# Performance work log

Hardware: AMD Instinct MI355X
Metric: run time of the kernel (lower is better)

The kernel has to match this reference:

```python
import jax, jax.numpy as jnp
import numpy as np

N_NODES = 100000
N_EDGES = 3200000
IN_DIM = 512
HEADS = 4
C1 = 8   # per-head channels, conv1
C2 = 4   # per-head channels, conv2
OUT_DIM = 10
NUM_GRAPHS = 64
NEG_SLOPE = 0.2  # PyG GATConv default


def setup_inputs() -> dict:
    key = jax.random.key(0)
    ks = jax.random.split(key, 16)
    s = lambda fan_in: 1.0 / np.sqrt(fan_in)
    inp = {
        "x": jax.random.normal(ks[0], (N_NODES, IN_DIM), jnp.float32),
        "edge_index": jax.random.randint(ks[1], (2, N_EDGES), 0, N_NODES, jnp.int32),
        "batch": jnp.sort(jax.random.randint(ks[2], (N_NODES,), 0, NUM_GRAPHS, jnp.int32)),
        # conv1 params
        "W1": jax.random.normal(ks[3], (IN_DIM, HEADS * C1), jnp.float32) * s(IN_DIM),
        "a1_src": jax.random.normal(ks[4], (HEADS, C1), jnp.float32) * s(C1),
        "a1_dst": jax.random.normal(ks[5], (HEADS, C1), jnp.float32) * s(C1),
        "b1": jnp.zeros((HEADS * C1,), jnp.float32),
        # conv2 params
        "W2": jax.random.normal(ks[6], (HEADS * C1, HEADS * C2), jnp.float32) * s(HEADS * C1),
        "a2_src": jax.random.normal(ks[7], (HEADS, C2), jnp.float32) * s(C2),
        "a2_dst": jax.random.normal(ks[8], (HEADS, C2), jnp.float32) * s(C2),
        "b2": jnp.zeros((HEADS * C2,), jnp.float32),
        # final linear
        "Wfc": jax.random.normal(ks[9], (HEADS * C2, OUT_DIM), jnp.float32) * s(HEADS * C2),
        "bfc": jnp.zeros((OUT_DIM,), jnp.float32),
    }
    return inp


def gat_conv(x, src, dst, W, a_src, a_dst, b):
    # x: [N, F]; src/dst: [E'] (self-loops already appended)
    N = x.shape[0]
    H, C = a_src.shape
    h = (x @ W).reshape(N, H, C)                      # per-node linear transform
    e_src = (h * a_src).sum(-1)                        # [N, H]
    e_dst = (h * a_dst).sum(-1)                        # [N, H]
    e = jax.nn.leaky_relu(e_src[src] + e_dst[dst], NEG_SLOPE)  # [E', H]
    # segment softmax over incoming edges of each destination node
    m = jax.ops.segment_max(e, dst, num_segments=N)    # [N, H]
    p = jnp.exp(e - m[dst])
    denom = jax.ops.segment_sum(p, dst, num_segments=N)
    alpha = p / denom[dst]                             # [E', H]
    out = jax.ops.segment_sum(h[src] * alpha[:, :, None], dst, num_segments=N)
    return out.reshape(N, H * C) + b


def reference(x, edge_index, batch, W1, a1_src, a1_dst, b1,
              W2, a2_src, a2_dst, b2, Wfc, bfc):
    N = x.shape[0]
    loops = jnp.arange(N, dtype=edge_index.dtype)      # PyG GATConv adds self-loops
    src = jnp.concatenate([edge_index[0], loops])
    dst = jnp.concatenate([edge_index[1], loops])

    h = jax.nn.relu(gat_conv(x, src, dst, W1, a1_src, a1_dst, b1))
    h = jax.nn.relu(gat_conv(h, src, dst, W2, a2_src, a2_dst, b2))

    # global mean pool over graph ids
    sums = jax.ops.segment_sum(h, batch, num_segments=NUM_GRAPHS)
    cnts = jax.ops.segment_sum(jnp.ones((N,), h.dtype), batch, num_segments=NUM_GRAPHS)
    pooled = sums / jnp.maximum(cnts, 1.0)[:, None]    # [G, H*C2]

    return pooled @ Wfc + bfc                          # [G, OUT_DIM]
```

## Files before the change

### kernel.cpp

```cpp
#include <hip/hip_runtime.h>
#include <hip/hip_bf16.h>

#define HEADS 4
#define NEG 0.2f
#define SHIFT 7
#define BKT 128

typedef float fv4 __attribute__((ext_vector_type(4)));
typedef unsigned short uv4 __attribute__((ext_vector_type(4)));
typedef unsigned short uv8 __attribute__((ext_vector_type(8)));

static __device__ __forceinline__ unsigned short f2bf(float f) {
  unsigned u = __float_as_uint(f);
  u += 0x7FFFu + ((u >> 16) & 1u);
  return (unsigned short)(u >> 16);
}
static __device__ __forceinline__ float bf2f(unsigned short h) {
  return __uint_as_float((unsigned)h << 16);
}

__global__ __launch_bounds__(256) void k_bin(const int* __restrict__ ei, int E,
                                             int K, int CAP,
                                             int* __restrict__ cursor,
                                             int* __restrict__ bins) {
  __shared__ int lcnt[1024];
  __shared__ int gbase[1024];
  const int t = threadIdx.x;
  const int nb = (E + 4095) >> 12;
  for (int batch = blockIdx.x; batch < nb; batch += gridDim.x) {
    const int e0 = batch << 12;
    for (int i = t; i < K; i += 256) lcnt[i] = 0;
    __syncthreads();
    int sreg[16], dreg[16], rank[16];
#pragma unroll
    for (int j = 0; j < 16; ++j) {
      int e = e0 + j * 256 + t;
      dreg[j] = -1;
      if (e < E) {
        sreg[j] = ei[e];
        dreg[j] = ei[E + e];
        rank[j] = atomicAdd(&lcnt[dreg[j] >> SHIFT], 1);
      }
    }
    __syncthreads();
    for (int i = t; i < K; i += 256)
      gbase[i] = (lcnt[i] > 0) ? atomicAdd(&cursor[i], lcnt[i]) : 0;
    __syncthreads();
#pragma unroll
    for (int j = 0; j < 16; ++j) {
      if (dreg[j] >= 0) {
        int b = dreg[j] >> SHIFT;
        int slot = gbase[b] + rank[j];
        if (slot < CAP)
          bins[(size_t)b * CAP + slot] = (sreg[j] << SHIFT) | (dreg[j] & (BKT - 1));
      }
    }
    __syncthreads();
  }
}

__global__ __launch_bounds__(256) void k_sort(int* __restrict__ bins,
                                              const int* __restrict__ cursor,
                                              int CAP, int N,
                                              int* __restrict__ rowbase,
                                              int* __restrict__ deg) {
  __shared__ int ebuf[6144];
  __shared__ int sbuf[6144];
  __shared__ int hist[BKT], pre[BKT], cur[BKT];
  const int b = blockIdx.x;
  const int base = b << SHIFT;
  const int t = threadIdx.x;
  int total = cursor[b]; if (total > CAP) total = CAP;
  int* gsrc = bins + (size_t)b * CAP;
  for (int i = t; i < total; i += 256) ebuf[i] = gsrc[i];
  if (t < BKT) hist[t] = 0;
  __syncthreads();
  for (int i = t; i < total; i += 256) atomicAdd(&hist[ebuf[i] & (BKT - 1)], 1);
  __syncthreads();
  if (t < BKT) pre[t] = hist[t];
  __syncthreads();
  for (int off = 1; off < BKT; off <<= 1) {
    int v = (t < BKT && t >= off) ? pre[t - off] : 0;
    __syncthreads();
    if (t < BKT) pre[t] += v;
    __syncthreads();
  }
  if (t < BKT) {
    int ex = pre[t] - hist[t];
    cur[t] = ex;
    int n = base + t;
    if (n < N) { rowbase[n] = b * CAP + ex; deg[n] = hist[t]; }
  }
  __syncthreads();
  for (int i = t; i < total; i += 256) {
    int pk = ebuf[i];
    int r = atomicAdd(&cur[pk & (BKT - 1)], 1);
    sbuf[r] = pk >> SHIFT;
  }
  __syncthreads();
  for (int i = t; i < total; i += 256) gsrc[i] = sbuf[i];
}

__global__ __launch_bounds__(256) void k_gemm1(const float* __restrict__ x,
                                               const float* __restrict__ W,
                                               const float* __restrict__ a1s,
                                               const float* __restrict__ a1d,
                                               unsigned short* __restrict__ g1b,
                                               float* __restrict__ e1s,
                                               float* __restrict__ e1d, int N) {
  __shared__ __align__(16) float xs[64][68];
  __shared__ __align__(16) float ws[64][32];
  const int t = threadIdx.x;
  const int n0 = blockIdx.x * 64;
  const int nl = t >> 2;
  const int cg = t & 3;
  float acc[8];
#pragma unroll
  for (int j = 0; j < 8; ++j) acc[j] = 0.f;
  const int r = t >> 4;
  const int kk = (t & 15) << 2;
  fv4 xr[4];
  float4 wr0, wr1;
#pragma unroll
  for (int i = 0; i < 4; ++i) {
    int gn = n0 + r + i * 16;
    fv4 v = {0.f, 0.f, 0.f, 0.f};
    if (gn < N) v = __builtin_nontemporal_load((const fv4*)(x + (size_t)gn * 512 + kk));
    xr[i] = v;
  }
  wr0 = ((const float4*)W)[t];
  wr1 = ((const float4*)W)[t + 256];
  for (int kc = 0; kc < 512; kc += 64) {
    __syncthreads();
#pragma unroll
    for (int i = 0; i < 4; ++i) *(fv4*)(&xs[r + i * 16][kk]) = xr[i];
    ((float4*)ws)[t] = wr0;
    ((float4*)ws)[t + 256] = wr1;
    __syncthreads();
    const int kn = kc + 64;
    if (kn < 512) {
#pragma unroll
      for (int i = 0; i < 4; ++i) {
        int gn = n0 + r + i * 16;
        fv4 v = {0.f, 0.f, 0.f, 0.f};
        if (gn < N) v = __builtin_nontemporal_load((const fv4*)(x + (size_t)gn * 512 + kn + kk));
        xr[i] = v;
      }
      wr0 = ((const float4*)(W + kn * 32))[t];
      wr1 = ((const float4*)(W + kn * 32))[t + 256];
    }
#pragma unroll
    for (int k = 0; k < 64; ++k) {
      float xv = xs[nl][k];
      float4 w0 = *(const float4*)(&ws[k][cg * 8]);
      float4 w1 = *(const float4*)(&ws[k][cg * 8 + 4]);
      acc[0] = fmaf(xv, w0.x, acc[0]);
      acc[1] = fmaf(xv, w0.y, acc[1]);
      acc[2] = fmaf(xv, w0.z, acc[2]);
      acc[3] = fmaf(xv, w0.w, acc[3]);
      acc[4] = fmaf(xv, w1.x, acc[4]);
      acc[5] = fmaf(xv, w1.y, acc[5]);
      acc[6] = fmaf(xv, w1.z, acc[6]);
      acc[7] = fmaf(xv, w1.w, acc[7]);
    }
  }
  int gn = n0 + nl;
  if (gn < N) {
    uv8 pk;
#pragma unroll
    for (int j = 0; j < 8; ++j) pk[j] = f2bf(acc[j]);
    *(uv8*)(g1b + (size_t)gn * 32 + cg * 8) = pk;
    const float* as = a1s + cg * 8;
    const float* ad = a1d + cg * 8;
    float s = 0.f, d = 0.f;
#pragma unroll
    for (int j = 0; j < 8; ++j) { s = fmaf(acc[j], as[j], s); d = fmaf(acc[j], ad[j], d); }
    e1s[gn * 4 + cg] = s;
    e1d[gn * 4 + cg] = d;
  }
}

__global__ __launch_bounds__(256) void k_agg1(const int* __restrict__ rowbase,
                                              const int* __restrict__ deg,
                                              const int* __restrict__ csr,
                                              const float* __restrict__ e1s,
                                              const float* __restrict__ e1d,
                                              const unsigned short* __restrict__ g1b,
                                              const float* __restrict__ b1,
                                              float* __restrict__ h1, int N) {
  int gid = blockIdx.x * blockDim.x + threadIdx.x;
  if (gid >= N * 8) return;
  int n = gid >> 3, cg = gid & 7, hd = cg >> 1;
  float edn = e1d[n * 4 + hd];
  float s = e1s[n * 4 + hd] + edn;
  float p = __expf(s > 0.f ? s : NEG * s);
  uv4 hv = *(const uv4*)(g1b + (size_t)n * 32 + cg * 4);
  float4 acc = make_float4(p * bf2f(hv.x), p * bf2f(hv.y), p * bf2f(hv.z), p * bf2f(hv.w));
  float den = p;
  int beg = rowbase[n], len = deg[n];
  const int* row = csr + beg;
  int i = 0;
  for (; i + 4 <= len; i += 4) {
    int s0 = row[i], s1 = row[i + 1], s2 = row[i + 2], s3 = row[i + 3];
    float ea = e1s[s0 * 4 + hd] + edn;
    float eb = e1s[s1 * 4 + hd] + edn;
    float ec = e1s[s2 * 4 + hd] + edn;
    float ed = e1s[s3 * 4 + hd] + edn;
    uv4 v0 = *(const uv4*)(g1b + (size_t)s0 * 32 + cg * 4);
    uv4 v1 = *(const uv4*)(g1b + (size_t)s1 * 32 + cg * 4);
    uv4 v2 = *(const uv4*)(g1b + (size_t)s2 * 32 + cg * 4);
    uv4 v3 = *(const uv4*)(g1b + (size_t)s3 * 32 + cg * 4);
    float p0 = __expf(ea > 0.f ? ea : NEG * ea);
    float p1 = __expf(eb > 0.f ? eb : NEG * eb);
    float p2 = __expf(ec > 0.f ? ec : NEG * ec);
    float p3 = __expf(ed > 0.f ? ed : NEG * ed);
    acc.x = fmaf(p0, bf2f(v0.x), acc.x);
    acc.y = fmaf(p0, bf2f(v0.y), acc.y);
    acc.z = fmaf(p0, bf2f(v0.z), acc.z);
    acc.w = fmaf(p0, bf2f(v0.w), acc.w);
    acc.x = fmaf(p1, bf2f(v1.x), acc.x);
    acc.y = fmaf(p1, bf2f(v1.y), acc.y);
    acc.z = fmaf(p1, bf2f(v1.z), acc.z);
    acc.w = fmaf(p1, bf2f(v1.w), acc.w);
    acc.x = fmaf(p2, bf2f(v2.x), acc.x);
    acc.y = fmaf(p2, bf2f(v2.y), acc.y);
    acc.z = fmaf(p2, bf2f(v2.z), acc.z);
    acc.w = fmaf(p2, bf2f(v2.w), acc.w);
    acc.x = fmaf(p3, bf2f(v3.x), acc.x);
    acc.y = fmaf(p3, bf2f(v3.y), acc.y);
    acc.z = fmaf(p3, bf2f(v3.z), acc.z);
    acc.w = fmaf(p3, bf2f(v3.w), acc.w);
    den += p0 + p1 + p2 + p3;
  }
  for (; i < len; ++i) {
    int s0 = row[i];
    float ea = e1s[s0 * 4 + hd] + edn;
    float p0 = __expf(ea > 0.f ? ea : NEG * ea);
    uv4 v0 = *(const uv4*)(g1b + (size_t)s0 * 32 + cg * 4);
    acc.x = fmaf(p0, bf2f(v0.x), acc.x);
    acc.y = fmaf(p0, bf2f(v0.y), acc.y);
    acc.z = fmaf(p0, bf2f(v0.z), acc.z);
    acc.w = fmaf(p0, bf2f(v0.w), acc.w);
    den += p0;
  }
  float inv = 1.f / den;
  const float* bp = b1 + cg * 4;
  float4 o;
  o.x = fmaxf(fmaf(acc.x, inv, bp[0]), 0.f);
  o.y = fmaxf(fmaf(acc.y, inv, bp[1]), 0.f);
  o.z = fmaxf(fmaf(acc.z, inv, bp[2]), 0.f);
  o.w = fmaxf(fmaf(acc.w, inv, bp[3]), 0.f);
  *(float4*)(h1 + (size_t)gid * 4) = o;
}

__global__ __launch_bounds__(256) void k_gemm2(const float* __restrict__ h1,
                                               const float* __restrict__ W2,
                                               const float* __restrict__ a2s_,
                                               const float* __restrict__ a2d_,
                                               unsigned short* __restrict__ g2b,
                                               float* __restrict__ e2s,
                                               float* __restrict__ e2d, int N) {
  __shared__ __align__(16) float hs[64][36];
  __shared__ __align__(16) float ws[32][16];
  const int t = threadIdx.x;
  const int n0 = blockIdx.x * 64;
  {
    int row = t >> 3, c4 = (t & 7) * 4;
#pragma unroll
    for (int i = 0; i < 2; ++i) {
      int rr = row + i * 32;
      int gn = n0 + rr;
      float4 v = make_float4(0.f, 0.f, 0.f, 0.f);
      if (gn < N) v = *(const float4*)(h1 + (size_t)gn * 32 + c4);
      *(float4*)(&hs[rr][c4]) = v;
    }
    if (t < 128) ((float4*)ws)[t] = ((const float4*)W2)[t];
  }
  __syncthreads();
  const int nl = t >> 2, cg = t & 3;
  float acc[4] = {0.f, 0.f, 0.f, 0.f};
#pragma unroll
  for (int k = 0; k < 32; ++k) {
    float xv = hs[nl][k];
    float4 w = *(const float4*)(&ws[k][cg * 4]);
    acc[0] = fmaf(xv, w.x, acc[0]);
    acc[1] = fmaf(xv, w.y, acc[1]);
    acc[2] = fmaf(xv, w.z, acc[2]);
    acc[3] = fmaf(xv, w.w, acc[3]);
  }
  int gn = n0 + nl;
  if (gn < N) {
    uv4 pk;
#pragma unroll
    for (int j = 0; j < 4; ++j) pk[j] = f2bf(acc[j]);
    *(uv4*)(g2b + (size_t)gn * 16 + cg * 4) = pk;
    const float* as = a2s_ + cg * 4;
    const float* ad = a2d_ + cg * 4;
    e2s[gn * 4 + cg] = acc[0] * as[0] + acc[1] * as[1] + acc[2] * as[2] + acc[3] * as[3];
    e2d[gn * 4 + cg] = acc[0] * ad[0] + acc[1] * ad[1] + acc[2] * ad[2] + acc[3] * ad[3];
  }
}

__global__ __launch_bounds__(256) void k_agg2(const int* __restrict__ rowbase,
                                              const int* __restrict__ deg,
                                              const int* __restrict__ csr,
                                              const float* __restrict__ e2s,
                                              const float* __restrict__ e2d,
                                              const unsigned short* __restrict__ g2b,
                                              const float* __restrict__ b2,
                                              float* __restrict__ h2, int N) {
  int gid = blockIdx.x * blockDim.x + threadIdx.x;
  if (gid >= N * 4) return;
  int n = gid >> 2, hd = gid & 3;
  float edn = e2d[n * 4 + hd];
  float s = e2s[n * 4 + hd] + edn;
  float p = __expf(s > 0.f ? s : NEG * s);
  uv4 hv = *(const uv4*)(g2b + (size_t)n * 16 + hd * 4);
  float4 acc = make_float4(p * bf2f(hv.x), p * bf2f(hv.y), p * bf2f(hv.z), p * bf2f(hv.w));
  float den = p;
  int beg = rowbase[n], len = deg[n];
  const int* row = csr + beg;
  int i = 0;
  for (; i + 4 <= len; i += 4) {
    int s0 = row[i], s1 = row[i + 1], s2 = row[i + 2], s3 = row[i + 3];
    float ea = e2s[s0 * 4 + hd] + edn;
    float eb = e2s[s1 * 4 + hd] + edn;
    float ec = e2s[s2 * 4 + hd] + edn;
    float ed = e2s[s3 * 4 + hd] + edn;
    uv4 v0 = *(const uv4*)(g2b + (size_t)s0 * 16 + hd * 4);
    uv4 v1 = *(const uv4*)(g2b + (size_t)s1 * 16 + hd * 4);
    uv4 v2 = *(const uv4*)(g2b + (size_t)s2 * 16 + hd * 4);
    uv4 v3 = *(const uv4*)(g2b + (size_t)s3 * 16 + hd * 4);
    float p0 = __expf(ea > 0.f ? ea : NEG * ea);
    float p1 = __expf(eb > 0.f ? eb : NEG * eb);
    float p2 = __expf(ec > 0.f ? ec : NEG * ec);
    float p3 = __expf(ed > 0.f ? ed : NEG * ed);
    acc.x = fmaf(p0, bf2f(v0.x), acc.x);
    acc.y = fmaf(p0, bf2f(v0.y), acc.y);
    acc.z = fmaf(p0, bf2f(v0.z), acc.z);
    acc.w = fmaf(p0, bf2f(v0.w), acc.w);
    acc.x = fmaf(p1, bf2f(v1.x), acc.x);
    acc.y = fmaf(p1, bf2f(v1.y), acc.y);
    acc.z = fmaf(p1, bf2f(v1.z), acc.z);
    acc.w = fmaf(p1, bf2f(v1.w), acc.w);
    acc.x = fmaf(p2, bf2f(v2.x), acc.x);
    acc.y = fmaf(p2, bf2f(v2.y), acc.y);
    acc.z = fmaf(p2, bf2f(v2.z), acc.z);
    acc.w = fmaf(p2, bf2f(v2.w), acc.w);
    acc.x = fmaf(p3, bf2f(v3.x), acc.x);
    acc.y = fmaf(p3, bf2f(v3.y), acc.y);
    acc.z = fmaf(p3, bf2f(v3.z), acc.z);
    acc.w = fmaf(p3, bf2f(v3.w), acc.w);
    den += p0 + p1 + p2 + p3;
  }
  for (; i < len; ++i) {
    int s0 = row[i];
    float ea = e2s[s0 * 4 + hd] + edn;
    float p0 = __expf(ea > 0.f ? ea : NEG * ea);
    uv4 v0 = *(const uv4*)(g2b + (size_t)s0 * 16 + hd * 4);
    acc.x = fmaf(p0, bf2f(v0.x), acc.x);
    acc.y = fmaf(p0, bf2f(v0.y), acc.y);
    acc.z = fmaf(p0, bf2f(v0.z), acc.z);
    acc.w = fmaf(p0, bf2f(v0.w), acc.w);
    den += p0;
  }
  float inv = 1.f / den;
  const float* bp = b2 + hd * 4;
  float4 o;
  o.x = fmaxf(fmaf(acc.x, inv, bp[0]), 0.f);
  o.y = fmaxf(fmaf(acc.y, inv, bp[1]), 0.f);
  o.z = fmaxf(fmaf(acc.z, inv, bp[2]), 0.f);
  o.w = fmaxf(fmaf(acc.w, inv, bp[3]), 0.f);
  *(float4*)(h2 + (size_t)gid * 4) = o;
}

__global__ __launch_bounds__(256) void k_poolfc(const float* __restrict__ h2,
                                                const int* __restrict__ batch,
                                                const float* __restrict__ Wfc,
                                                const float* __restrict__ bfc,
                                                float* __restrict__ out, int N) {
  __shared__ float ls[16][17];
  __shared__ float mean[16];
  __shared__ int bounds[2];
  const int g = blockIdx.x;
  const int t = threadIdx.x;
  if (t < 2) {
    int target = g + t;
    int lo = 0, hi = N;
    while (lo < hi) {
      int mid = (lo + hi) >> 1;
      if (batch[mid] < target) lo = mid + 1; else hi = mid;
    }
    bounds[t] = lo;
  }
  __syncthreads();
  const int start = bounds[0], end = bounds[1];
  const int c = t & 15, rg = t >> 4;
  float s = 0.f;
  for (int r = start + rg; r < end; r += 16) s += h2[(size_t)r * 16 + c];
  ls[rg][c] = s;
  __syncthreads();
  if (t < 16) {
    float sum = 0.f;
#pragma unroll
    for (int i = 0; i < 16; ++i) sum += ls[i][t];
    mean[t] = sum / fmaxf((float)(end - start), 1.f);
  }
  __syncthreads();
  if (t < 10) {
    float s2 = bfc[t];
#pragma unroll
    for (int k = 0; k < 16; ++k) s2 = fmaf(mean[k], Wfc[k * 10 + t], s2);
    out[g * 10 + t] = s2;
  }
}

extern "C" void kernel_launch(void* const* d_in, const int* in_sizes, int n_in,
                              void* d_out, int out_size, void* d_ws, size_t ws_size,
                              hipStream_t stream) {
  const float* x   = (const float*)d_in[0];
  const int*   ei  = (const int*)d_in[1];
  const int*   bat = (const int*)d_in[2];
  const float* W1  = (const float*)d_in[3];
  const float* a1s = (const float*)d_in[4];
  const float* a1d = (const float*)d_in[5];
  const float* b1  = (const float*)d_in[6];
  const float* W2  = (const float*)d_in[7];
  const float* a2s = (const float*)d_in[8];
  const float* a2d = (const float*)d_in[9];
  const float* b2  = (const float*)d_in[10];
  const float* Wfc = (const float*)d_in[11];
  const float* bfc = (const float*)d_in[12];
  const int N = in_sizes[2];
  const int E = in_sizes[1] / 2;

  float* ws = (float*)d_ws;
  unsigned short* g1b = (unsigned short*)ws;
  unsigned short* g2b = (unsigned short*)ws;
  float* e2s  = ws + (size_t)8 * N;
  float* e2d  = ws + (size_t)12 * N;
  float* e1s  = ws + (size_t)16 * N;
  float* e1d  = ws + (size_t)20 * N;
  float* h1   = ws + (size_t)24 * N;
  float* h2   = ws + (size_t)24 * N;
  int* cursor  = (int*)(ws + (size_t)56 * N);
  int* rowbase = cursor + 1024;
  int* deg     = rowbase + N;
  int* bins    = deg + N;

  const int K = (N + BKT - 1) >> SHIFT;
  long long availInts = (long long)(ws_size / 4) - 56LL * N - 1024 - 2LL * N;
  long long capLL = availInts / K;
  int CAP = (capLL > 6144) ? 6144 : (int)capLL;
  if (CAP < 1024) CAP = 1024;

  (void)hipMemsetAsync((void*)cursor, 0, 1024 * sizeof(int), stream);

  k_bin<<<512, 256, 0, stream>>>(ei, E, K, CAP, cursor, bins);
  k_sort<<<K, 256, 0, stream>>>(bins, cursor, CAP, N, rowbase, deg);
  k_gemm1<<<(N + 63) / 64, 256, 0, stream>>>(x, W1, a1s, a1d, g1b, e1s, e1d, N);
  k_agg1<<<(N * 8 + 255) / 256, 256, 0, stream>>>(rowbase, deg, bins, e1s, e1d, g1b, b1, h1, N);
  k_gemm2<<<(N + 63) / 64, 256, 0, stream>>>(h1, W2, a2s, a2d, g2b, e2s, e2d, N);
  k_agg2<<<(N * 4 + 255) / 256, 256, 0, stream>>>(rowbase, deg, bins, e2s, e2d, g2b, b2, h2, N);
  k_poolfc<<<64, 256, 0, stream>>>(h2, bat, Wfc, bfc, (float*)d_out, N);
}
```

Measured before the change: 304.2 us.

## Fuse layer-1 aggregation with layer-2 linear transform; one block per edge batch in binning

Layer-1 attention aggregation now feeds its ReLU output straight into shared memory, where the same block runs the 32x16 W2 projection and writes the bf16 g2 features and e2 attention scores. This removes the h1 round trip through global memory (N x 32 floats written and read back) and one kernel launch. Because layer 1 no longer shares buffers with layer 2, the workspace layout gives g2b, e2s and e2d their own regions. The binning kernel is also launched with one block per 4096-edge batch instead of a 512-block grid-stride loop. The fused kernel adds two block barriers and extra shared memory to the aggregation kernel, which may reduce occupancy.

```diff
diff --git a/kernel.cpp b/kernel.cpp
--- a/kernel.cpp
+++ b/kernel.cpp
@@ -26,36 +26,33 @@
   __shared__ int lcnt[1024];
   __shared__ int gbase[1024];
   const int t = threadIdx.x;
-  const int nb = (E + 4095) >> 12;
-  for (int batch = blockIdx.x; batch < nb; batch += gridDim.x) {
-    const int e0 = batch << 12;
-    for (int i = t; i < K; i += 256) lcnt[i] = 0;
-    __syncthreads();
-    int sreg[16], dreg[16], rank[16];
-#pragma unroll
-    for (int j = 0; j < 16; ++j) {
-      int e = e0 + j * 256 + t;
-      dreg[j] = -1;
-      if (e < E) {
-        sreg[j] = ei[e];
-        dreg[j] = ei[E + e];
-        rank[j] = atomicAdd(&lcnt[dreg[j] >> SHIFT], 1);
-      }
-    }
-    __syncthreads();
-    for (int i = t; i < K; i += 256)
-      gbase[i] = (lcnt[i] > 0) ? atomicAdd(&cursor[i], lcnt[i]) : 0;
-    __syncthreads();
-#pragma unroll
-    for (int j = 0; j < 16; ++j) {
-      if (dreg[j] >= 0) {
-        int b = dreg[j] >> SHIFT;
-        int slot = gbase[b] + rank[j];
-        if (slot < CAP)
-          bins[(size_t)b * CAP + slot] = (sreg[j] << SHIFT) | (dreg[j] & (BKT - 1));
-      }
-    }
-    __syncthreads();
+  const int batch = blockIdx.x;
+  const int e0 = batch << 12;
+  for (int i = t; i < K; i += 256) lcnt[i] = 0;
+  __syncthreads();
+  int sreg[16], dreg[16], rank[16];
+#pragma unroll
+  for (int j = 0; j < 16; ++j) {
+    int e = e0 + j * 256 + t;
+    dreg[j] = -1;
+    if (e < E) {
+      sreg[j] = ei[e];
+      dreg[j] = ei[E + e];
+      rank[j] = atomicAdd(&lcnt[dreg[j] >> SHIFT], 1);
+    }
+  }
+  __syncthreads();
+  for (int i = t; i < K; i += 256)
+    gbase[i] = (lcnt[i] > 0) ? atomicAdd(&cursor[i], lcnt[i]) : 0;
+  __syncthreads();
+#pragma unroll
+  for (int j = 0; j < 16; ++j) {
+    if (dreg[j] >= 0) {
+      int b = dreg[j] >> SHIFT;
+      int slot = gbase[b] + rank[j];
+      if (slot < CAP)
+        bins[(size_t)b * CAP + slot] = (sreg[j] << SHIFT) | (dreg[j] & (BKT - 1));
+    }
   }
 }
 
@@ -180,124 +177,113 @@
   }
 }
 
-__global__ __launch_bounds__(256) void k_agg1(const int* __restrict__ rowbase,
-                                              const int* __restrict__ deg,
-                                              const int* __restrict__ csr,
-                                              const float* __restrict__ e1s,
-                                              const float* __restrict__ e1d,
-                                              const unsigned short* __restrict__ g1b,
-                                              const float* __restrict__ b1,
-                                              float* __restrict__ h1, int N) {
-  int gid = blockIdx.x * blockDim.x + threadIdx.x;
-  if (gid >= N * 8) return;
-  int n = gid >> 3, cg = gid & 7, hd = cg >> 1;
-  float edn = e1d[n * 4 + hd];
-  float s = e1s[n * 4 + hd] + edn;
-  float p = __expf(s > 0.f ? s : NEG * s);
-  uv4 hv = *(const uv4*)(g1b + (size_t)n * 32 + cg * 4);
-  float4 acc = make_float4(p * bf2f(hv.x), p * bf2f(hv.y), p * bf2f(hv.z), p * bf2f(hv.w));
-  float den = p;
-  int beg = rowbase[n], len = deg[n];
-  const int* row = csr + beg;
-  int i = 0;
-  for (; i + 4 <= len; i += 4) {
-    int s0 = row[i], s1 = row[i + 1], s2 = row[i + 2], s3 = row[i + 3];
-    float ea = e1s[s0 * 4 + hd] + edn;
-    float eb = e1s[s1 * 4 + hd] + edn;
-    float ec = e1s[s2 * 4 + hd] + edn;
-    float ed = e1s[s3 * 4 + hd] + edn;
-    uv4 v0 = *(const uv4*)(g1b + (size_t)s0 * 32 + cg * 4);
-    uv4 v1 = *(const uv4*)(g1b + (size_t)s1 * 32 + cg * 4);
-    uv4 v2 = *(const uv4*)(g1b + (size_t)s2 * 32 + cg * 4);
-    uv4 v3 = *(const uv4*)(g1b + (size_t)s3 * 32 + cg * 4);
-    float p0 = __expf(ea > 0.f ? ea : NEG * ea);
-    float p1 = __expf(eb > 0.f ? eb : NEG * eb);
-    float p2 = __expf(ec > 0.f ? ec : NEG * ec);
-    float p3 = __expf(ed > 0.f ? ed : NEG * ed);
-    acc.x = fmaf(p0, bf2f(v0.x), acc.x);
-    acc.y = fmaf(p0, bf2f(v0.y), acc.y);
-    acc.z = fmaf(p0, bf2f(v0.z), acc.z);
-    acc.w = fmaf(p0, bf2f(v0.w), acc.w);
-    acc.x = fmaf(p1, bf2f(v1.x), acc.x);
-    acc.y = fmaf(p1, bf2f(v1.y), acc.y);
-    acc.z = fmaf(p1, bf2f(v1.z), acc.z);
-    acc.w = fmaf(p1, bf2f(v1.w), acc.w);
-    acc.x = fmaf(p2, bf2f(v2.x), acc.x);
-    acc.y = fmaf(p2, bf2f(v2.y), acc.y);
-    acc.z = fmaf(p2, bf2f(v2.z), acc.z);
-    acc.w = fmaf(p2, bf2f(v2.w), acc.w);
-    acc.x = fmaf(p3, bf2f(v3.x), acc.x);
-    acc.y = fmaf(p3, bf2f(v3.y), acc.y);
-    acc.z = fmaf(p3, bf2f(v3.z), acc.z);
-    acc.w = fmaf(p3, bf2f(v3.w), acc.w);
-    den += p0 + p1 + p2 + p3;
-  }
-  for (; i < len; ++i) {
-    int s0 = row[i];
-    float ea = e1s[s0 * 4 + hd] + edn;
-    float p0 = __expf(ea > 0.f ? ea : NEG * ea);
-    uv4 v0 = *(const uv4*)(g1b + (size_t)s0 * 32 + cg * 4);
-    acc.x = fmaf(p0, bf2f(v0.x), acc.x);
-    acc.y = fmaf(p0, bf2f(v0.y), acc.y);
-    acc.z = fmaf(p0, bf2f(v0.z), acc.z);
-    acc.w = fmaf(p0, bf2f(v0.w), acc.w);
-    den += p0;
-  }
-  float inv = 1.f / den;
-  const float* bp = b1 + cg * 4;
-  float4 o;
-  o.x = fmaxf(fmaf(acc.x, inv, bp[0]), 0.f);
-  o.y = fmaxf(fmaf(acc.y, inv, bp[1]), 0.f);
-  o.z = fmaxf(fmaf(acc.z, inv, bp[2]), 0.f);
-  o.w = fmaxf(fmaf(acc.w, inv, bp[3]), 0.f);
-  *(float4*)(h1 + (size_t)gid * 4) = o;
-}
-
-__global__ __launch_bounds__(256) void k_gemm2(const float* __restrict__ h1,
-                                               const float* __restrict__ W2,
-                                               const float* __restrict__ a2s_,
-                                               const float* __restrict__ a2d_,
-                                               unsigned short* __restrict__ g2b,
-                                               float* __restrict__ e2s,
-                                               float* __restrict__ e2d, int N) {
-  __shared__ __align__(16) float hs[64][36];
-  __shared__ __align__(16) float ws[32][16];
+__global__ __launch_bounds__(256) void k_agg1g2(
+    const int* __restrict__ rowbase, const int* __restrict__ deg,
+    const int* __restrict__ csr,
+    const float* __restrict__ e1s, const float* __restrict__ e1d,
+    const unsigned short* __restrict__ g1b, const float* __restrict__ b1,
+    const float* __restrict__ W2, const float* __restrict__ a2s_,
+    const float* __restrict__ a2d_,
+    unsigned short* __restrict__ g2b, float* __restrict__ e2s,
+    float* __restrict__ e2d, int N) {
+  __shared__ __align__(16) float h1s[32][36];
+  __shared__ __align__(16) float w2s[32][16];
+  __shared__ __align__(16) float g2s[32][20];
   const int t = threadIdx.x;
-  const int n0 = blockIdx.x * 64;
+  if (t < 128) ((float4*)w2s)[t] = ((const float4*)W2)[t];
+  const int gid = blockIdx.x * 256 + t;
+  const int n = gid >> 3, cg = gid & 7, hd = cg >> 1;
+  const int nl = t >> 3;
+  const bool valid = (n < N);
+  float4 o = make_float4(0.f, 0.f, 0.f, 0.f);
+  if (valid) {
+    float edn = e1d[n * 4 + hd];
+    float s = e1s[n * 4 + hd] + edn;
+    float p = __expf(s > 0.f ? s : NEG * s);
+    uv4 hv = *(const uv4*)(g1b + (size_t)n * 32 + cg * 4);
+    float4 acc = make_float4(p * bf2f(hv.x), p * bf2f(hv.y), p * bf2f(hv.z), p * bf2f(hv.w));
+    float den = p;
+    int beg = rowbase[n], len = deg[n];
+    const int* row = csr + beg;
+    int i = 0;
+    for (; i + 4 <= len; i += 4) {
+      int s0 = row[i], s1 = row[i + 1], s2 = row[i + 2], s3 = row[i + 3];
+      float ea = e1s[s0 * 4 + hd] + edn;
+      float eb = e1s[s1 * 4 + hd] + edn;
+      float ec = e1s[s2 * 4 + hd] + edn;
+      float ed = e1s[s3 * 4 + hd] + edn;
+      uv4 v0 = *(const uv4*)(g1b + (size_t)s0 * 32 + cg * 4);
+      uv4 v1 = *(const uv4*)(g1b + (size_t)s1 * 32 + cg * 4);
+      uv4 v2 = *(const uv4*)(g1b + (size_t)s2 * 32 + cg * 4);
+      uv4 v3 = *(const uv4*)(g1b + (size_t)s3 * 32 + cg * 4);
+      float p0 = __expf(ea > 0.f ? ea : NEG * ea);
+      float p1 = __expf(eb > 0.f ? eb : NEG * eb);
+      float p2 = __expf(ec > 0.f ? ec : NEG * ec);
+      float p3 = __expf(ed > 0.f ? ed : NEG * ed);
+      acc.x = fmaf(p0, bf2f(v0.x), acc.x);
+      acc.y = fmaf(p0, bf2f(v0.y), acc.y);
+      acc.z = fmaf(p0, bf2f(v0.z), acc.z);
+      acc.w = fmaf(p0, bf2f(v0.w), acc.w);
+      acc.x = fmaf(p1, bf2f(v1.x), acc.x);
+      acc.y = fmaf(p1, bf2f(v1.y), acc.y);
+      acc.z = fmaf(p1, bf2f(v1.z), acc.z);
+      acc.w = fmaf(p1, bf2f(v1.w), acc.w);
+      acc.x = fmaf(p2, bf2f(v2.x), acc.x);
+      acc.y = fmaf(p2, bf2f(v2.y), acc.y);
+      acc.z = fmaf(p2, bf2f(v2.z), acc.z);
+      acc.w = fmaf(p2, bf2f(v2.w), acc.w);
+      acc.x = fmaf(p3, bf2f(v3.x), acc.x);
+      acc.y = fmaf(p3, bf2f(v3.y), acc.y);
+      acc.z = fmaf(p3, bf2f(v3.z), acc.z);
+      acc.w = fmaf(p3, bf2f(v3.w), acc.w);
+      den += p0 + p1 + p2 + p3;
+    }
+    for (; i < len; ++i) {
+      int s0 = row[i];
+      float ea = e1s[s0 * 4 + hd] + edn;
+      float p0 = __expf(ea > 0.f ? ea : NEG * ea);
+      uv4 v0 = *(const uv4*)(g1b + (size_t)s0 * 32 + cg * 4);
+      acc.x = fmaf(p0, bf2f(v0.x), acc.x);
+      acc.y = fmaf(p0, bf2f(v0.y), acc.y);
+      acc.z = fmaf(p0, bf2f(v0.z), acc.z);
+      acc.w = fmaf(p0, bf2f(v0.w), acc.w);
+      den += p0;
+    }
+    float inv = 1.f / den;
+    const float* bp = b1 + cg * 4;
+    o.x = fmaxf(fmaf(acc.x, inv, bp[0]), 0.f);
+    o.y = fmaxf(fmaf(acc.y, inv, bp[1]), 0.f);
+    o.z = fmaxf(fmaf(acc.z, inv, bp[2]), 0.f);
+    o.w = fmaxf(fmaf(acc.w, inv, bp[3]), 0.f);
+  }
+  *(float4*)(&h1s[nl][cg * 4]) = o;
+  __syncthreads();
   {
-    int row = t >> 3, c4 = (t & 7) * 4;
-#pragma unroll
-    for (int i = 0; i < 2; ++i) {
-      int rr = row + i * 32;
-      int gn = n0 + rr;
-      float4 v = make_float4(0.f, 0.f, 0.f, 0.f);
-      if (gn < N) v = *(const float4*)(h1 + (size_t)gn * 32 + c4);
-      *(float4*)(&hs[rr][c4]) = v;
-    }
-    if (t < 128) ((float4*)ws)[t] = ((const float4*)W2)[t];
-  }
-  __syncthreads();
-  const int nl = t >> 2, cg = t & 3;
-  float acc[4] = {0.f, 0.f, 0.f, 0.f};
-#pragma unroll
-  for (int k = 0; k < 32; ++k) {
-    float xv = hs[nl][k];
-    float4 w = *(const float4*)(&ws[k][cg * 4]);
-    acc[0] = fmaf(xv, w.x, acc[0]);
-    acc[1] = fmaf(xv, w.y, acc[1]);
-    acc[2] = fmaf(xv, w.z, acc[2]);
-    acc[3] = fmaf(xv, w.w, acc[3]);
-  }
-  int gn = n0 + nl;
-  if (gn < N) {
-    uv4 pk;
-#pragma unroll
-    for (int j = 0; j < 4; ++j) pk[j] = f2bf(acc[j]);
-    *(uv4*)(g2b + (size_t)gn * 16 + cg * 4) = pk;
-    const float* as = a2s_ + cg * 4;
-    const float* ad = a2d_ + cg * 4;
-    e2s[gn * 4 + cg] = acc[0] * as[0] + acc[1] * as[1] + acc[2] * as[2] + acc[3] * as[3];
-    e2d[gn * 4 + cg] = acc[0] * ad[0] + acc[1] * ad[1] + acc[2] * ad[2] + acc[3] * ad[3];
+    const int c0 = (t & 7) * 2;
+    float a0 = 0.f, a1 = 0.f;
+#pragma unroll
+    for (int k = 0; k < 32; ++k) {
+      float hv = h1s[nl][k];
+      a0 = fmaf(hv, w2s[k][c0], a0);
+      a1 = fmaf(hv, w2s[k][c0 + 1], a1);
+    }
+    g2s[nl][c0] = a0;
+    g2s[nl][c0 + 1] = a1;
+  }
+  __syncthreads();
+  if (t < 128) {
+    int nl3 = t >> 2, h = t & 3;
+    int gn = blockIdx.x * 32 + nl3;
+    if (gn < N) {
+      float4 g = *(float4*)(&g2s[nl3][h * 4]);
+      uv4 pk;
+      pk[0] = f2bf(g.x); pk[1] = f2bf(g.y); pk[2] = f2bf(g.z); pk[3] = f2bf(g.w);
+      *(uv4*)(g2b + (size_t)gn * 16 + h * 4) = pk;
+      const float* as = a2s_ + h * 4;
+      const float* ad = a2d_ + h * 4;
+      e2s[gn * 4 + h] = g.x * as[0] + g.y * as[1] + g.z * as[2] + g.w * as[3];
+      e2d[gn * 4 + h] = g.x * ad[0] + g.y * ad[1] + g.z * ad[2] + g.w * ad[3];
+    }
   }
 }
 
@@ -436,13 +422,12 @@
 
   float* ws = (float*)d_ws;
   unsigned short* g1b = (unsigned short*)ws;
-  unsigned short* g2b = (unsigned short*)ws;
-  float* e2s  = ws + (size_t)8 * N;
-  float* e2d  = ws + (size_t)12 * N;
   float* e1s  = ws + (size_t)16 * N;
   float* e1d  = ws + (size_t)20 * N;
-  float* h1   = ws + (size_t)24 * N;
-  float* h2   = ws + (size_t)24 * N;
+  unsigned short* g2b = (unsigned short*)(ws + (size_t)24 * N);
+  float* e2s  = ws + (size_t)32 * N;
+  float* e2d  = ws + (size_t)36 * N;
+  float* h2   = ws + (size_t)40 * N;
   int* cursor  = (int*)(ws + (size_t)56 * N);
   int* rowbase = cursor + 1024;
   int* deg     = rowbase + N;
@@ -456,11 +441,13 @@
 
   (void)hipMemsetAsync((void*)cursor, 0, 1024 * sizeof(int), stream);
 
-  k_bin<<<512, 256, 0, stream>>>(ei, E, K, CAP, cursor, bins);
+  const int nb = (E + 4095) >> 12;
+  k_bin<<<nb, 256, 0, stream>>>(ei, E, K, CAP, cursor, bins);
   k_sort<<<K, 256, 0, stream>>>(bins, cursor, CAP, N, rowbase, deg);
   k_gemm1<<<(N + 63) / 64, 256, 0, stream>>>(x, W1, a1s, a1d, g1b, e1s, e1d, N);
-  k_agg1<<<(N * 8 + 255) / 256, 256, 0, stream>>>(rowbase, deg, bins, e1s, e1d, g1b, b1, h1, N);
-  k_gemm2<<<(N + 63) / 64, 256, 0, stream>>>(h1, W2, a2s, a2d, g2b, e2s, e2d, N);
+  k_agg1g2<<<(N * 8 + 255) / 256, 256, 0, stream>>>(rowbase, deg, bins, e1s, e1d,
+                                                    g1b, b1, W2, a2s, a2d,
+                                                    g2b, e2s, e2d, N);
   k_agg2<<<(N * 4 + 255) / 256, 256, 0, stream>>>(rowbase, deg, bins, e2s, e2d, g2b, b2, h2, N);
   k_poolfc<<<64, 256, 0, stream>>>(h2, bat, Wfc, bfc, (float*)d_out, N);
 }
```

Result: no change. 307.1 us (+0.9%).
